# Optimization experiments

Measured on AMD Instinct MI355X. Metric: run time of the kernel, lower is better.

Reference implementation:

```python
import jax, jax.numpy as jnp
import numpy as np

N, E, R, D, L, B, K = 50000, 800000, 64, 64, 4, 2, 32


def setup_inputs() -> dict:
    ks = jax.random.split(jax.random.key(0), 10)
    return {
        "edge_index": jax.random.randint(ks[0], (2, E), 0, N),
        "edge_type": jax.random.randint(ks[1], (E,), 0, R),
        "h_index": jax.random.randint(ks[2], (B,), 0, N),
        "r_index": jax.random.randint(ks[3], (B,), 0, R),
        "t_index": jax.random.randint(ks[4], (B, K), 0, N),
        "rel_repr": jax.random.normal(ks[5], (B, R, D)) * 0.1,
        "boundary_extra": jax.random.normal(ks[6], (B, N, D)) * 0.02,
        "layers_W": jax.random.normal(ks[7], (L, 2 * D, D)) / np.sqrt(2 * D),
        "layers_b": jnp.zeros((L, D)),
        "ln_g": jnp.ones((L, D)),
        "ln_b": jnp.zeros((L, D)),
        "w1": jax.random.normal(ks[8], (2 * D, D)) / np.sqrt(2 * D),
        "b1": jnp.zeros((D,)),
        "w2": jax.random.normal(ks[9], (D,)) / np.sqrt(D),
        "b2": jnp.zeros((1,)),
    }


def _layer_norm(x, g, b, eps=1e-5):
    mu = x.mean(-1, keepdims=True)
    var = ((x - mu) ** 2).mean(-1, keepdims=True)
    return (x - mu) * jax.lax.rsqrt(var + eps) * g + b


def reference(edge_index, edge_type, h_index, r_index, t_index, rel_repr,
              boundary_extra, layers_W, layers_b, ln_g, ln_b, w1, b1, w2, b2):
    src, dst = edge_index[0], edge_index[1]
    query = rel_repr[jnp.arange(B), r_index]  # [B, D] per-query relation embedding
    # enhanced boundary: entity/relation-enhanced base + query injected at head node
    boundary = boundary_extra.at[jnp.arange(B), h_index].add(query)  # [B, N, D]
    seg = jax.vmap(lambda m: jax.ops.segment_sum(m, dst, num_segments=N))
    x = boundary
    for l in range(L):
        msg = x[:, src, :] * rel_repr[:, edge_type, :]   # DistMult messages [B, E, D]
        agg = seg(msg) + boundary                        # sum aggregation + boundary self-message
        out = jnp.einsum('bnd,df->bnf', jnp.concatenate([x, agg], -1), layers_W[l]) + layers_b[l]
        out = jax.nn.relu(_layer_norm(out, ln_g[l], ln_b[l]))
        x = out + x                                      # short_cut residual
    node_feat = jnp.concatenate(
        [x, jnp.broadcast_to(query[:, None, :], (B, N, D))], axis=-1)  # [B, N, 2D]
    feat = node_feat[jnp.arange(B)[:, None], t_index]    # gather tails [B, K, 2D]
    h = jax.nn.relu(feat @ w1 + b1)
    score = h @ w2 + b2                                  # [B, K]
    return score
```

## Files before the change

kernel.cpp:

```cpp
#include <hip/hip_runtime.h>
#include <hip/hip_bf16.h>

#define NN 50000
#define EE 800000
#define RR 64
#define DD 64
#define LL 4
#define BB 2
#define KK 32

#define NBUK 98
#define BROWS 512
#define CHUNK 2048
#define NBLK 391
#define PLACE_CAP 10240
#define CAP3 8192

#define PREP_BLKS 196
#define INIT_BLKS 3125
#define HIST_BLKS 391

#define PB_REL   0
#define PB_WT    8192
#define PB_LB    40960
#define PB_G     41216
#define PB_BETA  41472
#define PB_W1    41728
#define PB_B1    49920
#define PB_W2    49984
#define PB_B2    50048
#define PB_TOT   50049

typedef short v8s __attribute__((ext_vector_type(8)));
typedef float v4f __attribute__((ext_vector_type(4)));
typedef _Float16 v2h __attribute__((ext_vector_type(2)));
typedef _Float16 v4h __attribute__((ext_vector_type(4)));
typedef _Float16 v8h __attribute__((ext_vector_type(8)));
typedef unsigned short v4u __attribute__((ext_vector_type(4)));

static __device__ __forceinline__ float ldany(const void* p, int i, int flag) {
    if (flag) return __bfloat162float(((const __hip_bfloat16*)p)[i]);
    return ((const float*)p)[i];
}
static __device__ __forceinline__ unsigned short tobf(float x) {
    return (unsigned short)(__builtin_bit_cast(unsigned int, x) >> 16);
}
static __device__ __forceinline__ unsigned short rnebf(float x) {
    unsigned int u = __builtin_bit_cast(unsigned int, x);
    return (unsigned short)((u + 0x7FFFu + ((u >> 16) & 1u)) >> 16);
}
static __device__ __forceinline__ float frombf(unsigned short h) {
    return __builtin_bit_cast(float, ((unsigned int)h) << 16);
}
static __device__ __forceinline__ int getflag(const unsigned int* lng) {
    return (*lng == 0x3F803F80u) ? 1 : 0;
}

__global__ void __launch_bounds__(256) k_prep(const void* __restrict__ rel, const void* __restrict__ lb,
                       const void* __restrict__ g, const void* __restrict__ beta,
                       const void* __restrict__ w1, const void* __restrict__ b1,
                       const void* __restrict__ w2, const void* __restrict__ b2,
                       const void* __restrict__ W, const unsigned int* __restrict__ lng,
                       const void* __restrict__ be,
                       const int* __restrict__ h_index, const int* __restrict__ r_index,
                       const int* __restrict__ ei,
                       float* __restrict__ pb, unsigned short* __restrict__ wshi,
                       unsigned short* __restrict__ wslo, _Float16* __restrict__ relH,
                       _Float16* __restrict__ xH, int* __restrict__ bucketCount) {
    __shared__ int h[NBUK];
    int blk = blockIdx.x, t = threadIdx.x;
    int flag = getflag(lng);

    if (blk >= PREP_BLKS + INIT_BLKS) {
        if (t < NBUK) h[t] = 0;
        __syncthreads();
        int base = (blk - PREP_BLKS - INIT_BLKS) * CHUNK;
        #pragma unroll
        for (int i = 0; i < 8; ++i) {
            int e = base + i * 256 + t;
            if (e < EE) atomicAdd(&h[ei[EE + e] >> 9], 1);
        }
        __syncthreads();
        if (t < NBUK && h[t]) atomicAdd(&bucketCount[t], h[t]);
        return;
    }
    if (blk >= PREP_BLKS) {
        int gid = (blk - PREP_BLKS) * 256 + t;
        int n = gid >> 4, j = gid & 15, d0 = j * 4;
        float x0[4], x1[4];
        if (flag) {
            v4u a = *(const v4u*)((const unsigned short*)be + (size_t)n * 64 + d0);
            v4u bq = *(const v4u*)((const unsigned short*)be + (size_t)(NN + n) * 64 + d0);
            #pragma unroll
            for (int jj = 0; jj < 4; ++jj) { x0[jj] = frombf(a[jj]); x1[jj] = frombf(bq[jj]); }
        } else {
            v4f a = *(const v4f*)((const float*)be + (size_t)n * 64 + d0);
            v4f bq = *(const v4f*)((const float*)be + (size_t)(NN + n) * 64 + d0);
            #pragma unroll
            for (int jj = 0; jj < 4; ++jj) { x0[jj] = a[jj]; x1[jj] = bq[jj]; }
        }
        if (n == h_index[0]) {
            int r = r_index[0];
            #pragma unroll
            for (int jj = 0; jj < 4; ++jj) x0[jj] += ldany(rel, r * DD + d0 + jj, flag);
        }
        if (n == h_index[1]) {
            int r = r_index[1];
            #pragma unroll
            for (int jj = 0; jj < 4; ++jj) x1[jj] += ldany(rel, (RR + r) * DD + d0 + jj, flag);
        }
        v8h o;
        #pragma unroll
        for (int jj = 0; jj < 4; ++jj) {
            o[2 * jj]     = (_Float16)x0[jj];
            o[2 * jj + 1] = (_Float16)x1[jj];
        }
        *(v8h*)(xH + (size_t)n * 128 + d0 * 2) = o;
        return;
    }

    int gid = blk * 256 + t;
    if (gid < 32768) {
        int l = gid >> 13, r = gid & 8191, f = r >> 7, d = r & 127;
        float w = ldany(W, l * 8192 + d * 64 + f, flag);
        unsigned short h2 = tobf(w);
        wshi[gid] = h2;
        wslo[gid] = tobf(w - frombf(h2));
        if (gid < 8192) {
            int ty = gid >> 7, rr = gid & 127, dd = rr >> 1, b = rr & 1;
            relH[gid] = (_Float16)ldany(rel, b * 4096 + ty * 64 + dd, flag);
        }
    }
    if (gid >= PB_TOT) return;
    if (gid < PB_WT) { pb[gid] = ldany(rel, gid, flag); return; }
    if (gid < PB_LB) return;
    if (gid < PB_G)    { pb[gid] = ldany(lb,   gid - PB_LB,   flag); return; }
    if (gid < PB_BETA) { pb[gid] = ldany(g,    gid - PB_G,    flag); return; }
    if (gid < PB_W1)   { pb[gid] = ldany(beta, gid - PB_BETA, flag); return; }
    if (gid < PB_B1)   { pb[gid] = ldany(w1,   gid - PB_W1,   flag); return; }
    if (gid < PB_W2)   { pb[gid] = ldany(b1,   gid - PB_B1,   flag); return; }
    if (gid < PB_B2)   { pb[gid] = ldany(w2,   gid - PB_W2,   flag); return; }
    pb[gid] = ldany(b2, 0, flag);
}

__global__ void __launch_bounds__(256) k_bfill(const int* __restrict__ ei,
                                               const int* __restrict__ et,
                                               const int* __restrict__ bucketCount,
                                               int* __restrict__ bcur,
                                               unsigned int* __restrict__ btmp) {
    __shared__ int h[NBUK], rb[NBUK], sb[128];
    int t = threadIdx.x;
    int v = 0;
    if (t < 128) { v = (t < NBUK) ? bucketCount[t] : 0; sb[t] = v; }
    __syncthreads();
    for (int off = 1; off < 128; off <<= 1) {
        int a = (t < 128 && t >= off) ? sb[t - off] : 0;
        __syncthreads();
        if (t < 128 && t >= off) sb[t] += a;
        __syncthreads();
    }
    if (t < NBUK) sb[t] -= v;
    if (t < NBUK) h[t] = 0;
    __syncthreads();
    int base = blockIdx.x * CHUNK;
    unsigned int rec[8]; int bk[8];
    #pragma unroll
    for (int i = 0; i < 8; ++i) {
        int e = base + i * 256 + t;
        bk[i] = -1;
        if (e < EE) {
            int dst = ei[EE + e];
            rec[i] = (unsigned int)ei[e] | ((unsigned int)et[e] << 16)
                   | ((unsigned int)(dst & 511) << 22);
            bk[i] = dst >> 9;
            atomicAdd(&h[bk[i]], 1);
        }
    }
    __syncthreads();
    if (t < NBUK) rb[t] = h[t] ? (sb[t] + atomicAdd(&bcur[t], h[t])) : 0;
    __syncthreads();
    if (t < NBUK) h[t] = 0;
    __syncthreads();
    #pragma unroll
    for (int i = 0; i < 8; ++i) {
        if (bk[i] >= 0) {
            int pos = rb[bk[i]] + atomicAdd(&h[bk[i]], 1);
            btmp[pos] = rec[i];
        }
    }
}

__global__ void __launch_bounds__(256) k_place(const int* __restrict__ bucketCount,
                                               const unsigned int* __restrict__ btmp,
                                               unsigned int* __restrict__ elist,
                                               int* __restrict__ rowptr) {
    __shared__ int rp[BROWS + 1];
    __shared__ int cur[BROWS];
    __shared__ unsigned int outb[PLACE_CAP];
    __shared__ int sb[128];
    __shared__ int s_base, s_cnt;
    int b = blockIdx.x, t = threadIdx.x;
    int v = 0;
    if (t < 128) { v = (t < NBUK) ? bucketCount[t] : 0; sb[t] = v; }
    __syncthreads();
    for (int off = 1; off < 128; off <<= 1) {
        int a = (t < 128 && t >= off) ? sb[t - off] : 0;
        __syncthreads();
        if (t < 128 && t >= off) sb[t] += a;
        __syncthreads();
    }
    if (t == 0) { int cb = bucketCount[b]; s_base = sb[b] - cb; s_cnt = cb; }
    __syncthreads();
    int base = s_base;
    int cnt  = s_cnt;

    for (int r = t; r < BROWS; r += 256) cur[r] = 0;
    __syncthreads();
    for (int i = t; i < cnt; i += 256) {
        unsigned int rec = btmp[base + i];
        atomicAdd(&cur[rec >> 22], 1);
    }
    __syncthreads();
    if (t < 64) {
        int lane = t;
        int loc[8]; int s = 0;
        #pragma unroll
        for (int j = 0; j < 8; ++j) { loc[j] = s; s += cur[lane * 8 + j]; }
        int inc = s;
        for (int off = 1; off < 64; off <<= 1) {
            int vv = __shfl_up(inc, off, 64);
            if (lane >= off) inc += vv;
        }
        int excl = inc - s;
        #pragma unroll
        for (int j = 0; j < 8; ++j) rp[lane * 8 + j] = excl + loc[j];
        if (lane == 63) rp[BROWS] = inc;
    }
    __syncthreads();
    for (int r = t; r < BROWS; r += 256) cur[r] = rp[r];
    __syncthreads();
    for (int i = t; i < cnt; i += 256) {
        unsigned int rec = btmp[base + i];
        int ld = rec >> 22;
        int pos = atomicAdd(&cur[ld], 1);
        outb[pos] = rec & 0x3FFFFFu;
    }
    __syncthreads();
    for (int i = t; i < cnt; i += 256) elist[base + i] = outb[i];
    for (int r = t; r < BROWS; r += 256) {
        int n = b * BROWS + r;
        if (n <= NN) rowptr[n] = base + rp[r];
    }
}

__global__ void k_sets(const int* __restrict__ t_index,
                       const int* __restrict__ rowptr,
                       const unsigned int* __restrict__ elist,
                       int* __restrict__ flag3,
                       int* __restrict__ listT, int* __restrict__ posT,
                       int* __restrict__ list3, int* __restrict__ cnts) {
    __shared__ int sT, s3;
    __shared__ int lT[64];
    int t = threadIdx.x;
    if (t == 0) { sT = 0; s3 = 0; }
    __syncthreads();
    if (t < 64) {
        int n = t_index[t];
        if (atomicExch(&flag3[n], 1) == 0) {
            int p = atomicAdd(&sT, 1);
            lT[p] = n; listT[p] = n; list3[p] = n;
        }
    }
    __syncthreads();
    int nT = sT;
    if (t == 0) s3 = nT;
    __syncthreads();
    if (t < 64) {
        int n = t_index[t];
        int p = 0;
        for (int j = 0; j < nT; ++j) { if (lT[j] == n) { p = j; break; } }
        posT[t] = p;
    }
    int wave = t >> 6, lane = t & 63;
    for (int idx = wave; idx < nT; idx += 4) {
        int n = lT[idx];
        int s0 = rowptr[n], s1 = rowptr[n + 1];
        for (int i = s0 + lane; i < s1; i += 64) {
            int src = (int)(elist[i] & 0xFFFFu);
            if (atomicExch(&flag3[src], 1) == 0) {
                int p = atomicAdd(&s3, 1);
                if (p < CAP3) list3[p] = src;
            }
        }
    }
    __syncthreads();
    if (t == 0) { cnts[0] = nT; cnts[1] = (s3 > CAP3) ? CAP3 : s3; }
}

__global__ void __launch_bounds__(256) k_set2(const int* __restrict__ rowptr,
                                              const unsigned int* __restrict__ elist,
                                              const int* __restrict__ list3,
                                              const int* __restrict__ cnt3,
                                              int* __restrict__ flag2,
                                              int* __restrict__ list2,
                                              int* __restrict__ cnt2) {
    int wave = threadIdx.x >> 6, lane = threadIdx.x & 63;
    int nw = gridDim.x * 4;
    int c3 = *cnt3;
    for (int idx = blockIdx.x * 4 + wave; idx < c3; idx += nw) {
        int n = list3[idx];
        if (lane == 0) {
            if (atomicExch(&flag2[n], 1) == 0) list2[atomicAdd(cnt2, 1)] = n;
        }
        int s0 = rowptr[n], s1 = rowptr[n + 1];
        for (int i = s0 + lane; i < s1; i += 64) {
            int src = (int)(elist[i] & 0xFFFFu);
            if (atomicExch(&flag2[src], 1) == 0) {
                list2[atomicAdd(cnt2, 1)] = src;
            }
        }
    }
}

__global__ void __launch_bounds__(256) k_gather(const int* __restrict__ rowptr,
                                                const unsigned int* __restrict__ elist,
                                                const _Float16* __restrict__ xHin,
                                                const _Float16* __restrict__ relH,
                                                const void* __restrict__ be,
                                                const float* __restrict__ relf,
                                                const int* __restrict__ h_index,
                                                const int* __restrict__ r_index,
                                                const unsigned int* __restrict__ lng,
                                                const int* __restrict__ list,
                                                const int* __restrict__ cntp,
                                                unsigned short* __restrict__ aggH) {
    int wave = threadIdx.x >> 6, lane = threadIdx.x & 63;
    int idx = blockIdx.x * 4 + wave;
    int cnt = cntp ? *cntp : NN;
    if (idx >= cnt) return;
    int n = list ? list[idx] : idx;
    n = __builtin_amdgcn_readfirstlane(n);
    int start = __builtin_amdgcn_readfirstlane(rowptr[n]);
    int end   = __builtin_amdgcn_readfirstlane(rowptr[n + 1]);
    int flag  = getflag(lng);

    float a0 = ldany(be, n * DD + lane, flag);
    float a1 = ldany(be, (NN + n) * DD + lane, flag);
    if (n == h_index[0]) a0 += relf[(0 * RR + r_index[0]) * DD + lane];
    if (n == h_index[1]) a1 += relf[(1 * RR + r_index[1]) * DD + lane];

    for (int i = start; i < end; i += 8) {
        v2h xv[8], rv[8]; float mk[8];
        #pragma unroll
        for (int j = 0; j < 8; ++j) {
            int e = i + j;
            int ok = (e < end);
            unsigned int u = elist[ok ? e : start];
            int s = u & 0xFFFFu, ty = u >> 16;
            xv[j] = *(const v2h*)(xHin + s * 128 + lane * 2);
            rv[j] = *(const v2h*)(relH + ty * 128 + lane * 2);
            mk[j] = ok ? 1.f : 0.f;
        }
        #pragma unroll
        for (int j = 0; j < 8; ++j) {
            a0 += (float)xv[j].x * (float)rv[j].x * mk[j];
            a1 += (float)xv[j].y * (float)rv[j].y * mk[j];
        }
    }
    aggH[n * 64 + lane] = rnebf(a0);
    aggH[(NN + n) * 64 + lane] = rnebf(a1);
}

__global__ void __launch_bounds__(256) k_combine(const _Float16* __restrict__ xHin,
                                                 const unsigned short* __restrict__ aggH,
                                                 const unsigned short* __restrict__ whi,
                                                 const unsigned short* __restrict__ wlo,
                                                 const float* __restrict__ lb,
                                                 const float* __restrict__ g,
                                                 const float* __restrict__ beta,
                                                 const int* __restrict__ list,
                                                 const int* __restrict__ cntp,
                                                 _Float16* __restrict__ xHout) {
    __shared__ __attribute__((aligned(16))) unsigned short Xhi[64 * 136];
    __shared__ __attribute__((aligned(16))) unsigned short Xlo[64 * 72];
    __shared__ int nodes[32];
    float* outT = (float*)Xhi;

    int t = threadIdx.x;
    int cnt = cntp ? *cntp : NN;
    int ebase = blockIdx.x * 32;
    if (ebase >= cnt) return;

    if (t < 32) {
        int e = ebase + t;
        int ce = e < cnt ? e : cnt - 1;
        nodes[t] = list ? list[ce] : ce;
    }
    __syncthreads();

    #pragma unroll
    for (int it = 0; it < 4; ++it) {
        int idx = it * 256 + t;
        int nl = idx >> 5, j = idx & 31;
        int n = nodes[nl];
        v4h v = *(const v4h*)(xHin + (size_t)n * 128 + 4 * j);
        int r0 = nl, r1 = 32 + nl;
        int k0 = 2 * j, k1 = 2 * j + 1;
        float f; unsigned short h;
        f = (float)v.x; h = tobf(f); Xhi[r0 * 136 + k0] = h; Xlo[r0 * 72 + k0] = tobf(f - frombf(h));
        f = (float)v.y; h = tobf(f); Xhi[r1 * 136 + k0] = h; Xlo[r1 * 72 + k0] = tobf(f - frombf(h));
        f = (float)v.z; h = tobf(f); Xhi[r0 * 136 + k1] = h; Xlo[r0 * 72 + k1] = tobf(f - frombf(h));
        f = (float)v.w; h = tobf(f); Xhi[r1 * 136 + k1] = h; Xlo[r1 * 72 + k1] = tobf(f - frombf(h));
    }
    #pragma unroll
    for (int it = 0; it < 4; ++it) {
        int idx = it * 256 + t;
        int half = idx >> 9, rem = idx & 511;
        int nl = rem >> 4, j = rem & 15;
        int n = nodes[nl];
        v4u v = *(const v4u*)(aggH + (size_t)(half * NN + n) * 64 + 4 * j);
        int row = half * 32 + nl;
        int kb = 64 + 4 * j;
        Xhi[row * 136 + kb + 0] = v.x;
        Xhi[row * 136 + kb + 1] = v.y;
        Xhi[row * 136 + kb + 2] = v.z;
        Xhi[row * 136 + kb + 3] = v.w;
    }
    __syncthreads();

    int wave = t >> 6, lane = t & 63;
    int low = lane & 15, q = lane >> 4;

    v4f acc[4];
    #pragma unroll
    for (int ft = 0; ft < 4; ++ft) acc[ft] = 0.f;

    int arow = wave * 16 + low;
    #pragma unroll
    for (int kt = 0; kt < 2; ++kt) {
        int k0 = kt * 32 + q * 8;
        v8s ah = *(const v8s*)(Xhi + arow * 136 + k0);
        v8s al = *(const v8s*)(Xlo + arow * 72 + k0);
        #pragma unroll
        for (int ft = 0; ft < 4; ++ft) {
            v8s bh = *(const v8s*)(whi + (ft * 16 + low) * 128 + k0);
            v8s bl = *(const v8s*)(wlo + (ft * 16 + low) * 128 + k0);
            acc[ft] = __builtin_amdgcn_mfma_f32_16x16x32_bf16(ah, bh, acc[ft], 0, 0, 0);
            acc[ft] = __builtin_amdgcn_mfma_f32_16x16x32_bf16(al, bh, acc[ft], 0, 0, 0);
            acc[ft] = __builtin_amdgcn_mfma_f32_16x16x32_bf16(ah, bl, acc[ft], 0, 0, 0);
        }
    }
    #pragma unroll
    for (int kt = 2; kt < 4; ++kt) {
        int k0 = kt * 32 + q * 8;
        v8s ah = *(const v8s*)(Xhi + arow * 136 + k0);
        #pragma unroll
        for (int ft = 0; ft < 4; ++ft) {
            v8s bh = *(const v8s*)(whi + (ft * 16 + low) * 128 + k0);
            v8s bl = *(const v8s*)(wlo + (ft * 16 + low) * 128 + k0);
            acc[ft] = __builtin_amdgcn_mfma_f32_16x16x32_bf16(ah, bh, acc[ft], 0, 0, 0);
            acc[ft] = __builtin_amdgcn_mfma_f32_16x16x32_bf16(ah, bl, acc[ft], 0, 0, 0);
        }
    }

    float o[4][4];
    #pragma unroll
    for (int ft = 0; ft < 4; ++ft) {
        float lbv = lb[ft * 16 + low];
        #pragma unroll
        for (int r = 0; r < 4; ++r) o[ft][r] = acc[ft][r] + lbv;
    }
    float s1[4], s2[4];
    #pragma unroll
    for (int r = 0; r < 4; ++r) {
        s1[r] = o[0][r] + o[1][r] + o[2][r] + o[3][r];
        s2[r] = o[0][r]*o[0][r] + o[1][r]*o[1][r] + o[2][r]*o[2][r] + o[3][r]*o[3][r];
    }
    #pragma unroll
    for (int m = 1; m < 16; m <<= 1) {
        #pragma unroll
        for (int r = 0; r < 4; ++r) {
            s1[r] += __shfl_xor(s1[r], m, 64);
            s2[r] += __shfl_xor(s2[r], m, 64);
        }
    }
    float res[4][4];
    #pragma unroll
    for (int r = 0; r < 4; ++r) {
        int row = wave * 16 + q * 4 + r;
        float mu  = s1[r] * (1.f / 64.f);
        float var = s2[r] * (1.f / 64.f) - mu * mu;
        float rs  = rsqrtf(fmaxf(var, 0.f) + 1e-5f);
        #pragma unroll
        for (int ft = 0; ft < 4; ++ft) {
            int f = ft * 16 + low;
            float xold = frombf(Xhi[row * 136 + f]) + frombf(Xlo[row * 72 + f]);
            res[ft][r] = fmaxf((o[ft][r] - mu) * rs * g[f] + beta[f], 0.f) + xold;
        }
    }
    __syncthreads();

    #pragma unroll
    for (int r = 0; r < 4; ++r) {
        int row = wave * 16 + q * 4 + r;
        #pragma unroll
        for (int ft = 0; ft < 4; ++ft) outT[row * 65 + ft * 16 + low] = res[ft][r];
    }
    __syncthreads();

    #pragma unroll
    for (int it = 0; it < 4; ++it) {
        int idx = it * 256 + t;
        int nl = idx >> 5, j = idx & 31;
        if (ebase + nl < cnt) {
            int n = nodes[nl];
            v4h hv;
            hv.x = (_Float16)outT[nl * 65 + 2 * j];
            hv.y = (_Float16)outT[(32 + nl) * 65 + 2 * j];
            hv.z = (_Float16)outT[nl * 65 + 2 * j + 1];
            hv.w = (_Float16)outT[(32 + nl) * 65 + 2 * j + 1];
            *(v4h*)(xHout + (size_t)n * 128 + 4 * j) = hv;
        }
    }
}

__global__ void __launch_bounds__(256) k_tail(const int* __restrict__ rowptr,
                                              const unsigned int* __restrict__ elist,
                                              const _Float16* __restrict__ xHin,
                                              const _Float16* __restrict__ relH,
                                              const void* __restrict__ be,
                                              const float* __restrict__ pb,
                                              const int* __restrict__ h_index,
                                              const int* __restrict__ r_index,
                                              const unsigned int* __restrict__ lng,
                                              const int* __restrict__ listT,
                                              const int* __restrict__ posT,
                                              const int* __restrict__ cnts,
                                              const unsigned short* __restrict__ whi,
                                              const unsigned short* __restrict__ wlo,
                                              const float* __restrict__ lb,
                                              const float* __restrict__ g,
                                              const float* __restrict__ beta,
                                              void* __restrict__ out) {
    __shared__ __attribute__((aligned(16))) unsigned short Xhi[64 * 136];
    __shared__ __attribute__((aligned(16))) unsigned short Xlo[64 * 72];
    __shared__ int nodes[32];
    float* outT = (float*)Xhi;

    int t = threadIdx.x;
    int wave = t >> 6, lane = t & 63;
    int cntT = cnts[0];
    int ebase = blockIdx.x * 32;
    if (ebase >= cntT) return;
    int flag = getflag(lng);
    const float* relf = pb + PB_REL;
    int h0 = h_index[0], h1 = h_index[1];
    int ri0 = r_index[0], ri1 = r_index[1];

    if (t < 32) {
        int e = ebase + t;
        int ce = e < cntT ? e : cntT - 1;
        nodes[t] = listT[ce];
    }
    __syncthreads();

    #pragma unroll
    for (int it = 0; it < 4; ++it) {
        int idx = it * 256 + t;
        int nl = idx >> 5, j = idx & 31;
        int n = nodes[nl];
        v4h v = *(const v4h*)(xHin + (size_t)n * 128 + 4 * j);
        int r0 = nl, r1 = 32 + nl;
        int k0 = 2 * j, k1 = 2 * j + 1;
        float f; unsigned short h;
        f = (float)v.x; h = tobf(f); Xhi[r0 * 136 + k0] = h; Xlo[r0 * 72 + k0] = tobf(f - frombf(h));
        f = (float)v.y; h = tobf(f); Xhi[r1 * 136 + k0] = h; Xlo[r1 * 72 + k0] = tobf(f - frombf(h));
        f = (float)v.z; h = tobf(f); Xhi[r0 * 136 + k1] = h; Xlo[r0 * 72 + k1] = tobf(f - frombf(h));
        f = (float)v.w; h = tobf(f); Xhi[r1 * 136 + k1] = h; Xlo[r1 * 72 + k1] = tobf(f - frombf(h));
    }

    #pragma unroll 1
    for (int kk = 0; kk < 8; ++kk) {
        int nl = wave * 8 + kk;
        if (ebase + nl < cntT) {
            int n = __builtin_amdgcn_readfirstlane(nodes[nl]);
            int start = __builtin_amdgcn_readfirstlane(rowptr[n]);
            int end   = __builtin_amdgcn_readfirstlane(rowptr[n + 1]);
            float a0 = ldany(be, n * DD + lane, flag);
            float a1 = ldany(be, (NN + n) * DD + lane, flag);
            if (n == h0) a0 += relf[ri0 * DD + lane];
            if (n == h1) a1 += relf[(RR + ri1) * DD + lane];
            for (int i = start; i < end; i += 8) {
                v2h xv[8], rv[8]; float mk[8];
                #pragma unroll
                for (int j = 0; j < 8; ++j) {
                    int e = i + j;
                    int ok = (e < end);
                    unsigned int u = elist[ok ? e : start];
                    int s = u & 0xFFFFu, ty = u >> 16;
                    xv[j] = *(const v2h*)(xHin + s * 128 + lane * 2);
                    rv[j] = *(const v2h*)(relH + ty * 128 + lane * 2);
                    mk[j] = ok ? 1.f : 0.f;
                }
                #pragma unroll
                for (int j = 0; j < 8; ++j) {
                    a0 += (float)xv[j].x * (float)rv[j].x * mk[j];
                    a1 += (float)xv[j].y * (float)rv[j].y * mk[j];
                }
            }
            Xhi[nl * 136 + 64 + lane] = rnebf(a0);
            Xhi[(32 + nl) * 136 + 64 + lane] = rnebf(a1);
        } else {
            Xhi[nl * 136 + 64 + lane] = 0;
            Xhi[(32 + nl) * 136 + 64 + lane] = 0;
        }
    }
    __syncthreads();

    int low = lane & 15, q = lane >> 4;
    v4f acc[4];
    #pragma unroll
    for (int ft = 0; ft < 4; ++ft) acc[ft] = 0.f;
    int arow = wave * 16 + low;
    #pragma unroll
    for (int kt = 0; kt < 2; ++kt) {
        int k0 = kt * 32 + q * 8;
        v8s ah = *(const v8s*)(Xhi + arow * 136 + k0);
        v8s al = *(const v8s*)(Xlo + arow * 72 + k0);
        #pragma unroll
        for (int ft = 0; ft < 4; ++ft) {
            v8s bh = *(const v8s*)(whi + (ft * 16 + low) * 128 + k0);
            v8s bl = *(const v8s*)(wlo + (ft * 16 + low) * 128 + k0);
            acc[ft] = __builtin_amdgcn_mfma_f32_16x16x32_bf16(ah, bh, acc[ft], 0, 0, 0);
            acc[ft] = __builtin_amdgcn_mfma_f32_16x16x32_bf16(al, bh, acc[ft], 0, 0, 0);
            acc[ft] = __builtin_amdgcn_mfma_f32_16x16x32_bf16(ah, bl, acc[ft], 0, 0, 0);
        }
    }
    #pragma unroll
    for (int kt = 2; kt < 4; ++kt) {
        int k0 = kt * 32 + q * 8;
        v8s ah = *(const v8s*)(Xhi + arow * 136 + k0);
        #pragma unroll
        for (int ft = 0; ft < 4; ++ft) {
            v8s bh = *(const v8s*)(whi + (ft * 16 + low) * 128 + k0);
            v8s bl = *(const v8s*)(wlo + (ft * 16 + low) * 128 + k0);
            acc[ft] = __builtin_amdgcn_mfma_f32_16x16x32_bf16(ah, bh, acc[ft], 0, 0, 0);
            acc[ft] = __builtin_amdgcn_mfma_f32_16x16x32_bf16(ah, bl, acc[ft], 0, 0, 0);
        }
    }
    float o[4][4];
    #pragma unroll
    for (int ft = 0; ft < 4; ++ft) {
        float lbv = lb[ft * 16 + low];
        #pragma unroll
        for (int r = 0; r < 4; ++r) o[ft][r] = acc[ft][r] + lbv;
    }
    float s1[4], s2[4];
    #pragma unroll
    for (int r = 0; r < 4; ++r) {
        s1[r] = o[0][r] + o[1][r] + o[2][r] + o[3][r];
        s2[r] = o[0][r]*o[0][r] + o[1][r]*o[1][r] + o[2][r]*o[2][r] + o[3][r]*o[3][r];
    }
    #pragma unroll
    for (int m = 1; m < 16; m <<= 1) {
        #pragma unroll
        for (int r = 0; r < 4; ++r) {
            s1[r] += __shfl_xor(s1[r], m, 64);
            s2[r] += __shfl_xor(s2[r], m, 64);
        }
    }
    float res[4][4];
    #pragma unroll
    for (int r = 0; r < 4; ++r) {
        int row = wave * 16 + q * 4 + r;
        float mu  = s1[r] * (1.f / 64.f);
        float var = s2[r] * (1.f / 64.f) - mu * mu;
        float rs  = rsqrtf(fmaxf(var, 0.f) + 1e-5f);
        #pragma unroll
        for (int ft = 0; ft < 4; ++ft) {
            int f = ft * 16 + low;
            float xold = frombf(Xhi[row * 136 + f]) + frombf(Xlo[row * 72 + f]);
            res[ft][r] = fmaxf((o[ft][r] - mu) * rs * g[f] + beta[f], 0.f) + xold;
        }
    }
    __syncthreads();
    #pragma unroll
    for (int r = 0; r < 4; ++r) {
        int row = wave * 16 + q * 4 + r;
        #pragma unroll
        for (int ft = 0; ft < 4; ++ft) outT[row * 65 + ft * 16 + low] = res[ft][r];
    }
    __syncthreads();

    const float* w1 = pb + PB_W1;
    for (int j = wave; j < BB * KK; j += 4) {
        int pj = posT[j];
        if (pj >= ebase && pj < ebase + 32) {
            int b = j >> 5, k = j & 31;
            int row = b * 32 + (pj - ebase);
            const float* qv = relf + (b * RR + ((b == 0) ? ri0 : ri1)) * DD;
            float acc2 = pb[PB_B1 + lane];
            #pragma unroll 8
            for (int d = 0; d < 64; ++d) acc2 += outT[row * 65 + d] * w1[d * 64 + lane];
            #pragma unroll 8
            for (int d = 0; d < 64; ++d) acc2 += qv[d] * w1[(64 + d) * 64 + lane];
            float hh = fmaxf(acc2, 0.f);
            float p = hh * pb[PB_W2 + lane];
            for (int m = 32; m > 0; m >>= 1) p += __shfl_xor(p, m, 64);
            if (lane == 0) {
                float s = p + pb[PB_B2];
                if (flag) ((__hip_bfloat16*)out)[b * KK + k] = __float2bfloat16(s);
                else      ((float*)out)[b * KK + k] = s;
            }
        }
    }
}

extern "C" void kernel_launch(void* const* d_in, const int* in_sizes, int n_in,
                              void* d_out, int out_size, void* d_ws, size_t ws_size,
                              hipStream_t stream) {
    const int* edge_index = (const int*)d_in[0];
    const int* edge_type  = (const int*)d_in[1];
    const int* h_index    = (const int*)d_in[2];
    const int* r_index    = (const int*)d_in[3];
    const int* t_index    = (const int*)d_in[4];
    const void* rel   = d_in[5];
    const void* be    = d_in[6];
    const void* lw    = d_in[7];
    const void* lbias = d_in[8];
    const void* lng   = d_in[9];
    const void* lnb   = d_in[10];
    const void* w1    = d_in[11];
    const void* b1    = d_in[12];
    const void* w2    = d_in[13];
    const void* b2    = d_in[14];

    _Float16* xHa = (_Float16*)d_ws;
    _Float16* xHb = xHa + (size_t)NN * 128;
    unsigned short* aggH = (unsigned short*)(xHb + (size_t)NN * 128);
    float*    pb  = (float*)(aggH + (size_t)BB * NN * 64);
    int*      ip  = (int*)(pb + PB_TOT);
    int* bucketCount = ip;
    int* bcur   = bucketCount + NBUK;
    int* flag2  = bcur + NBUK;
    int* flag3  = flag2 + NN;
    int* cnts   = flag3 + NN;
    int* rowptr = cnts + 16;
    int* listT  = rowptr + NN + 1;
    int* posT   = listT + 64;
    int* list3  = posT + 64;
    int* list2  = list3 + CAP3;
    unsigned int* elist = (unsigned int*)(list2 + NN);
    unsigned short* wshi = (unsigned short*)(elist + EE);
    unsigned short* wslo = wshi + 32768;
    _Float16* relH = (_Float16*)(wslo + 32768);
    unsigned int* btmp = (unsigned int*)xHb;
    const unsigned int* lngp = (const unsigned int*)lng;

    hipMemsetAsync(bucketCount, 0, (size_t)(2 * NBUK + 2 * NN + 16) * sizeof(int), stream);
    k_prep<<<PREP_BLKS + INIT_BLKS + HIST_BLKS, 256, 0, stream>>>(
        rel, lbias, lng, lnb, w1, b1, w2, b2, lw, lngp, be, h_index, r_index,
        edge_index, pb, wshi, wslo, relH, xHa, bucketCount);
    k_bfill<<<NBLK, 256, 0, stream>>>(edge_index, edge_type, bucketCount, bcur, btmp);
    k_place<<<NBUK, 256, 0, stream>>>(bucketCount, btmp, elist, rowptr);
    k_sets<<<1, 256, 0, stream>>>(t_index, rowptr, elist, flag3, listT, posT, list3, cnts);
    k_set2<<<256, 256, 0, stream>>>(rowptr, elist, list3, cnts + 1, flag2, list2, cnts + 2);

    const float* relf = pb + PB_REL;
    k_gather<<<12500, 256, 0, stream>>>(rowptr, elist, xHa, relH, be, relf,
                                        h_index, r_index, lngp, nullptr, nullptr, aggH);
    k_combine<<<1563, 256, 0, stream>>>(xHa, aggH, wshi + 0, wslo + 0,
                                        pb + PB_LB + 0, pb + PB_G + 0, pb + PB_BETA + 0,
                                        nullptr, nullptr, xHb);
    k_gather<<<12500, 256, 0, stream>>>(rowptr, elist, xHb, relH, be, relf,
                                        h_index, r_index, lngp, list2, cnts + 2, aggH);
    k_combine<<<1563, 256, 0, stream>>>(xHb, aggH, wshi + 8192, wslo + 8192,
                                        pb + PB_LB + 64, pb + PB_G + 64, pb + PB_BETA + 64,
                                        list2, cnts + 2, xHa);
    k_gather<<<2048, 256, 0, stream>>>(rowptr, elist, xHa, relH, be, relf,
                                       h_index, r_index, lngp, list3, cnts + 1, aggH);
    k_combine<<<256, 256, 0, stream>>>(xHa, aggH, wshi + 16384, wslo + 16384,
                                       pb + PB_LB + 128, pb + PB_G + 128, pb + PB_BETA + 128,
                                       list3, cnts + 1, xHb);
    k_tail<<<2, 256, 0, stream>>>(rowptr, elist, xHb, relH, be, pb,
                                  h_index, r_index, lngp, listT, posT, cnts,
                                  wshi + 24576, wslo + 24576,
                                  pb + PB_LB + 192, pb + PB_G + 192, pb + PB_BETA + 192,
                                  d_out);
}
```

Measured before the change: 377.9 us.

## Fuse layer-3 gather and combine into one kernel, spread tail over more blocks

Replaces the separate layer-3 gather and combine launches with one templated kernel, k_gc. Each wave aggregates one node and then applies the linear layer, layernorm and residual on the CUDA cores, using split bf16 hi/lo weights. The final-layer tail uses the same kernel with 4 nodes per block over 16 blocks instead of 32 nodes per block over 2 blocks, so the small tail gets more parallelism. The intent is to remove one launch and the round trip of the aggregation buffer through global memory. In exchange it gives up the MFMA matmul for a scalar FMA loop and leans on the sets being small.

```diff
diff --git a/kernel.cpp b/kernel.cpp
--- a/kernel.cpp
+++ b/kernel.cpp
@@ -524,193 +524,147 @@
     }
 }
 
-__global__ void __launch_bounds__(256) k_tail(const int* __restrict__ rowptr,
-                                              const unsigned int* __restrict__ elist,
-                                              const _Float16* __restrict__ xHin,
-                                              const _Float16* __restrict__ relH,
-                                              const void* __restrict__ be,
-                                              const float* __restrict__ pb,
-                                              const int* __restrict__ h_index,
-                                              const int* __restrict__ r_index,
-                                              const unsigned int* __restrict__ lng,
-                                              const int* __restrict__ listT,
-                                              const int* __restrict__ posT,
-                                              const int* __restrict__ cnts,
-                                              const unsigned short* __restrict__ whi,
-                                              const unsigned short* __restrict__ wlo,
-                                              const float* __restrict__ lb,
-                                              const float* __restrict__ g,
-                                              const float* __restrict__ beta,
-                                              void* __restrict__ out) {
-    __shared__ __attribute__((aligned(16))) unsigned short Xhi[64 * 136];
-    __shared__ __attribute__((aligned(16))) unsigned short Xlo[64 * 72];
-    __shared__ int nodes[32];
-    float* outT = (float*)Xhi;
-
-    int t = threadIdx.x;
-    int wave = t >> 6, lane = t & 63;
-    int cntT = cnts[0];
-    int ebase = blockIdx.x * 32;
-    if (ebase >= cntT) return;
+template<int FINAL>
+__global__ void __launch_bounds__(256) k_gc(const int* __restrict__ rowptr,
+                                            const unsigned int* __restrict__ elist,
+                                            const _Float16* __restrict__ xHin,
+                                            const _Float16* __restrict__ relH,
+                                            const void* __restrict__ be,
+                                            const float* __restrict__ pb,
+                                            const int* __restrict__ h_index,
+                                            const int* __restrict__ r_index,
+                                            const unsigned int* __restrict__ lng,
+                                            const int* __restrict__ list,
+                                            const int* __restrict__ cntp,
+                                            const unsigned short* __restrict__ whi,
+                                            const unsigned short* __restrict__ wlo,
+                                            const float* __restrict__ lb,
+                                            const float* __restrict__ g,
+                                            const float* __restrict__ beta,
+                                            _Float16* __restrict__ xHout,
+                                            const int* __restrict__ posT,
+                                            void* __restrict__ out) {
+    __shared__ float xrow[8][64];
+    __shared__ float aggL[8][64];
+    __shared__ float resL[8][64];
+    int t = threadIdx.x, wave = t >> 6, lane = t & 63;
+    int cnt = *cntp;
+    int ebase = blockIdx.x * 4;
+    if (ebase >= cnt) return;
+    int idx = ebase + wave;
     int flag = getflag(lng);
     const float* relf = pb + PB_REL;
-    int h0 = h_index[0], h1 = h_index[1];
-    int ri0 = r_index[0], ri1 = r_index[1];
-
-    if (t < 32) {
-        int e = ebase + t;
-        int ce = e < cntT ? e : cntT - 1;
-        nodes[t] = listT[ce];
-    }
-    __syncthreads();
-
-    #pragma unroll
-    for (int it = 0; it < 4; ++it) {
-        int idx = it * 256 + t;
-        int nl = idx >> 5, j = idx & 31;
-        int n = nodes[nl];
-        v4h v = *(const v4h*)(xHin + (size_t)n * 128 + 4 * j);
-        int r0 = nl, r1 = 32 + nl;
-        int k0 = 2 * j, k1 = 2 * j + 1;
-        float f; unsigned short h;
-        f = (float)v.x; h = tobf(f); Xhi[r0 * 136 + k0] = h; Xlo[r0 * 72 + k0] = tobf(f - frombf(h));
-        f = (float)v.y; h = tobf(f); Xhi[r1 * 136 + k0] = h; Xlo[r1 * 72 + k0] = tobf(f - frombf(h));
-        f = (float)v.z; h = tobf(f); Xhi[r0 * 136 + k1] = h; Xlo[r0 * 72 + k1] = tobf(f - frombf(h));
-        f = (float)v.w; h = tobf(f); Xhi[r1 * 136 + k1] = h; Xlo[r1 * 72 + k1] = tobf(f - frombf(h));
-    }
-
-    #pragma unroll 1
-    for (int kk = 0; kk < 8; ++kk) {
-        int nl = wave * 8 + kk;
-        if (ebase + nl < cntT) {
-            int n = __builtin_amdgcn_readfirstlane(nodes[nl]);
-            int start = __builtin_amdgcn_readfirstlane(rowptr[n]);
-            int end   = __builtin_amdgcn_readfirstlane(rowptr[n + 1]);
-            float a0 = ldany(be, n * DD + lane, flag);
-            float a1 = ldany(be, (NN + n) * DD + lane, flag);
-            if (n == h0) a0 += relf[ri0 * DD + lane];
-            if (n == h1) a1 += relf[(RR + ri1) * DD + lane];
-            for (int i = start; i < end; i += 8) {
-                v2h xv[8], rv[8]; float mk[8];
-                #pragma unroll
-                for (int j = 0; j < 8; ++j) {
-                    int e = i + j;
-                    int ok = (e < end);
-                    unsigned int u = elist[ok ? e : start];
-                    int s = u & 0xFFFFu, ty = u >> 16;
-                    xv[j] = *(const v2h*)(xHin + s * 128 + lane * 2);
-                    rv[j] = *(const v2h*)(relH + ty * 128 + lane * 2);
-                    mk[j] = ok ? 1.f : 0.f;
+    int active = (idx < cnt);
+
+    int n = -1;
+    float xa = 0.f, xb = 0.f, a0 = 0.f, a1 = 0.f;
+    if (active) {
+        n = __builtin_amdgcn_readfirstlane(list[idx]);
+        int start = __builtin_amdgcn_readfirstlane(rowptr[n]);
+        int end   = __builtin_amdgcn_readfirstlane(rowptr[n + 1]);
+        v2h xv2 = *(const v2h*)(xHin + (size_t)n * 128 + lane * 2);
+        xa = (float)xv2.x; xb = (float)xv2.y;
+        a0 = ldany(be, n * DD + lane, flag);
+        a1 = ldany(be, (NN + n) * DD + lane, flag);
+        if (n == h_index[0]) a0 += relf[(0 * RR + r_index[0]) * DD + lane];
+        if (n == h_index[1]) a1 += relf[(1 * RR + r_index[1]) * DD + lane];
+        for (int i = start; i < end; i += 8) {
+            v2h xv[8], rv[8]; float mk[8];
+            #pragma unroll
+            for (int j = 0; j < 8; ++j) {
+                int e = i + j;
+                int ok = (e < end);
+                unsigned int u = elist[ok ? e : start];
+                int s = u & 0xFFFFu, ty = u >> 16;
+                xv[j] = *(const v2h*)(xHin + s * 128 + lane * 2);
+                rv[j] = *(const v2h*)(relH + ty * 128 + lane * 2);
+                mk[j] = ok ? 1.f : 0.f;
+            }
+            #pragma unroll
+            for (int j = 0; j < 8; ++j) {
+                a0 += (float)xv[j].x * (float)rv[j].x * mk[j];
+                a1 += (float)xv[j].y * (float)rv[j].y * mk[j];
+            }
+        }
+        a0 = frombf(rnebf(a0));
+        a1 = frombf(rnebf(a1));
+    }
+    xrow[wave * 2 + 0][lane] = xa;
+    xrow[wave * 2 + 1][lane] = xb;
+    aggL[wave * 2 + 0][lane] = a0;
+    aggL[wave * 2 + 1][lane] = a1;
+    __syncthreads();
+
+    int f = lane;
+    int r0 = wave * 2, r1 = wave * 2 + 1;
+    float d0 = lb[f], d1 = d0;
+    for (int k0 = 0; k0 < 64; k0 += 8) {
+        v8s wh = *(const v8s*)(whi + f * 128 + k0);
+        v8s wl = *(const v8s*)(wlo + f * 128 + k0);
+        #pragma unroll
+        for (int j = 0; j < 8; ++j) {
+            float wv = frombf((unsigned short)wh[j]) + frombf((unsigned short)wl[j]);
+            d0 += xrow[r0][k0 + j] * wv;
+            d1 += xrow[r1][k0 + j] * wv;
+        }
+    }
+    for (int k0 = 64; k0 < 128; k0 += 8) {
+        v8s wh = *(const v8s*)(whi + f * 128 + k0);
+        v8s wl = *(const v8s*)(wlo + f * 128 + k0);
+        #pragma unroll
+        for (int j = 0; j < 8; ++j) {
+            float wv = frombf((unsigned short)wh[j]) + frombf((unsigned short)wl[j]);
+            d0 += aggL[r0][k0 + j - 64] * wv;
+            d1 += aggL[r1][k0 + j - 64] * wv;
+        }
+    }
+    float s1a = d0, s2a = d0 * d0, s1b = d1, s2b = d1 * d1;
+    #pragma unroll
+    for (int m = 1; m < 64; m <<= 1) {
+        s1a += __shfl_xor(s1a, m, 64);
+        s2a += __shfl_xor(s2a, m, 64);
+        s1b += __shfl_xor(s1b, m, 64);
+        s2b += __shfl_xor(s2b, m, 64);
+    }
+    float mua = s1a * (1.f / 64.f);
+    float vara = s2a * (1.f / 64.f) - mua * mua;
+    float rsa = rsqrtf(fmaxf(vara, 0.f) + 1e-5f);
+    float mub = s1b * (1.f / 64.f);
+    float varb = s2b * (1.f / 64.f) - mub * mub;
+    float rsb = rsqrtf(fmaxf(varb, 0.f) + 1e-5f);
+    float gv = g[f], bv = beta[f];
+    float res0 = fmaxf((d0 - mua) * rsa * gv + bv, 0.f) + xa;
+    float res1 = fmaxf((d1 - mub) * rsb * gv + bv, 0.f) + xb;
+
+    if (active) {
+        v2h hv; hv.x = (_Float16)res0; hv.y = (_Float16)res1;
+        *(v2h*)(xHout + (size_t)n * 128 + lane * 2) = hv;
+    }
+
+    if (FINAL) {
+        resL[r0][lane] = res0;
+        resL[r1][lane] = res1;
+        __syncthreads();
+        const float* w1 = pb + PB_W1;
+        for (int j = wave; j < BB * KK; j += 4) {
+            int pj = posT[j];
+            if (pj >= ebase && pj < ebase + 4) {
+                int b = j >> 5, k = j & 31;
+                int row = (pj - ebase) * 2 + b;
+                const float* qv = relf + (b * RR + r_index[b]) * DD;
+                float acc2 = pb[PB_B1 + lane];
+                #pragma unroll 8
+                for (int d = 0; d < 64; ++d) acc2 += resL[row][d] * w1[d * 64 + lane];
+                #pragma unroll 8
+                for (int d = 0; d < 64; ++d) acc2 += qv[d] * w1[(64 + d) * 64 + lane];
+                float hh = fmaxf(acc2, 0.f);
+                float p = hh * pb[PB_W2 + lane];
+                for (int m = 32; m > 0; m >>= 1) p += __shfl_xor(p, m, 64);
+                if (lane == 0) {
+                    float s = p + pb[PB_B2];
+                    if (flag) ((__hip_bfloat16*)out)[b * KK + k] = __float2bfloat16(s);
+                    else      ((float*)out)[b * KK + k] = s;
                 }
-                #pragma unroll
-                for (int j = 0; j < 8; ++j) {
-                    a0 += (float)xv[j].x * (float)rv[j].x * mk[j];
-                    a1 += (float)xv[j].y * (float)rv[j].y * mk[j];
-                }
-            }
-            Xhi[nl * 136 + 64 + lane] = rnebf(a0);
-            Xhi[(32 + nl) * 136 + 64 + lane] = rnebf(a1);
-        } else {
-            Xhi[nl * 136 + 64 + lane] = 0;
-            Xhi[(32 + nl) * 136 + 64 + lane] = 0;
-        }
-    }
-    __syncthreads();
-
-    int low = lane & 15, q = lane >> 4;
-    v4f acc[4];
-    #pragma unroll
-    for (int ft = 0; ft < 4; ++ft) acc[ft] = 0.f;
-    int arow = wave * 16 + low;
-    #pragma unroll
-    for (int kt = 0; kt < 2; ++kt) {
-        int k0 = kt * 32 + q * 8;
-        v8s ah = *(const v8s*)(Xhi + arow * 136 + k0);
-        v8s al = *(const v8s*)(Xlo + arow * 72 + k0);
-        #pragma unroll
-        for (int ft = 0; ft < 4; ++ft) {
-            v8s bh = *(const v8s*)(whi + (ft * 16 + low) * 128 + k0);
-            v8s bl = *(const v8s*)(wlo + (ft * 16 + low) * 128 + k0);
-            acc[ft] = __builtin_amdgcn_mfma_f32_16x16x32_bf16(ah, bh, acc[ft], 0, 0, 0);
-            acc[ft] = __builtin_amdgcn_mfma_f32_16x16x32_bf16(al, bh, acc[ft], 0, 0, 0);
-            acc[ft] = __builtin_amdgcn_mfma_f32_16x16x32_bf16(ah, bl, acc[ft], 0, 0, 0);
-        }
-    }
-    #pragma unroll
-    for (int kt = 2; kt < 4; ++kt) {
-        int k0 = kt * 32 + q * 8;
-        v8s ah = *(const v8s*)(Xhi + arow * 136 + k0);
-        #pragma unroll
-        for (int ft = 0; ft < 4; ++ft) {
-            v8s bh = *(const v8s*)(whi + (ft * 16 + low) * 128 + k0);
-            v8s bl = *(const v8s*)(wlo + (ft * 16 + low) * 128 + k0);
-            acc[ft] = __builtin_amdgcn_mfma_f32_16x16x32_bf16(ah, bh, acc[ft], 0, 0, 0);
-            acc[ft] = __builtin_amdgcn_mfma_f32_16x16x32_bf16(ah, bl, acc[ft], 0, 0, 0);
-        }
-    }
-    float o[4][4];
-    #pragma unroll
-    for (int ft = 0; ft < 4; ++ft) {
-        float lbv = lb[ft * 16 + low];
-        #pragma unroll
-        for (int r = 0; r < 4; ++r) o[ft][r] = acc[ft][r] + lbv;
-    }
-    float s1[4], s2[4];
-    #pragma unroll
-    for (int r = 0; r < 4; ++r) {
-        s1[r] = o[0][r] + o[1][r] + o[2][r] + o[3][r];
-        s2[r] = o[0][r]*o[0][r] + o[1][r]*o[1][r] + o[2][r]*o[2][r] + o[3][r]*o[3][r];
-    }
-    #pragma unroll
-    for (int m = 1; m < 16; m <<= 1) {
-        #pragma unroll
-        for (int r = 0; r < 4; ++r) {
-            s1[r] += __shfl_xor(s1[r], m, 64);
-            s2[r] += __shfl_xor(s2[r], m, 64);
-        }
-    }
-    float res[4][4];
-    #pragma unroll
-    for (int r = 0; r < 4; ++r) {
-        int row = wave * 16 + q * 4 + r;
-        float mu  = s1[r] * (1.f / 64.f);
-        float var = s2[r] * (1.f / 64.f) - mu * mu;
-        float rs  = rsqrtf(fmaxf(var, 0.f) + 1e-5f);
-        #pragma unroll
-        for (int ft = 0; ft < 4; ++ft) {
-            int f = ft * 16 + low;
-            float xold = frombf(Xhi[row * 136 + f]) + frombf(Xlo[row * 72 + f]);
-            res[ft][r] = fmaxf((o[ft][r] - mu) * rs * g[f] + beta[f], 0.f) + xold;
-        }
-    }
-    __syncthreads();
-    #pragma unroll
-    for (int r = 0; r < 4; ++r) {
-        int row = wave * 16 + q * 4 + r;
-        #pragma unroll
-        for (int ft = 0; ft < 4; ++ft) outT[row * 65 + ft * 16 + low] = res[ft][r];
-    }
-    __syncthreads();
-
-    const float* w1 = pb + PB_W1;
-    for (int j = wave; j < BB * KK; j += 4) {
-        int pj = posT[j];
-        if (pj >= ebase && pj < ebase + 32) {
-            int b = j >> 5, k = j & 31;
-            int row = b * 32 + (pj - ebase);
-            const float* qv = relf + (b * RR + ((b == 0) ? ri0 : ri1)) * DD;
-            float acc2 = pb[PB_B1 + lane];
-            #pragma unroll 8
-            for (int d = 0; d < 64; ++d) acc2 += outT[row * 65 + d] * w1[d * 64 + lane];
-            #pragma unroll 8
-            for (int d = 0; d < 64; ++d) acc2 += qv[d] * w1[(64 + d) * 64 + lane];
-            float hh = fmaxf(acc2, 0.f);
-            float p = hh * pb[PB_W2 + lane];
-            for (int m = 32; m > 0; m >>= 1) p += __shfl_xor(p, m, 64);
-            if (lane == 0) {
-                float s = p + pb[PB_B2];
-                if (flag) ((__hip_bfloat16*)out)[b * KK + k] = __float2bfloat16(s);
-                else      ((float*)out)[b * KK + k] = s;
             }
         }
     }
@@ -777,14 +731,14 @@
     k_combine<<<1563, 256, 0, stream>>>(xHb, aggH, wshi + 8192, wslo + 8192,
                                         pb + PB_LB + 64, pb + PB_G + 64, pb + PB_BETA + 64,
                                         list2, cnts + 2, xHa);
-    k_gather<<<2048, 256, 0, stream>>>(rowptr, elist, xHa, relH, be, relf,
-                                       h_index, r_index, lngp, list3, cnts + 1, aggH);
-    k_combine<<<256, 256, 0, stream>>>(xHa, aggH, wshi + 16384, wslo + 16384,
-                                       pb + PB_LB + 128, pb + PB_G + 128, pb + PB_BETA + 128,
-                                       list3, cnts + 1, xHb);
-    k_tail<<<2, 256, 0, stream>>>(rowptr, elist, xHb, relH, be, pb,
-                                  h_index, r_index, lngp, listT, posT, cnts,
-                                  wshi + 24576, wslo + 24576,
-                                  pb + PB_LB + 192, pb + PB_G + 192, pb + PB_BETA + 192,
-                                  d_out);
-}
+    k_gc<0><<<2048, 256, 0, stream>>>(rowptr, elist, xHa, relH, be, pb,
+                                      h_index, r_index, lngp, list3, cnts + 1,
+                                      wshi + 16384, wslo + 16384,
+                                      pb + PB_LB + 128, pb + PB_G + 128, pb + PB_BETA + 128,
+                                      xHb, nullptr, nullptr);
+    k_gc<1><<<16, 256, 0, stream>>>(rowptr, elist, xHb, relH, be, pb,
+                                    h_index, r_index, lngp, listT, cnts + 0,
+                                    wshi + 24576, wslo + 24576,
+                                    pb + PB_LB + 192, pb + PB_G + 192, pb + PB_BETA + 192,
+                                    xHa, posT, d_out);
+}
```

After: 336.1 us. -11.1%, faster.
